# Performance work log

Hardware: AMD Instinct MI355X
Metric: run time of the kernel (lower is better)

The kernel has to match this reference:

```python
import jax, jax.numpy as jnp
import numpy as np

NUM_PTS = 1024
LATENT_SIZE = 32
BETA = 0.1


def setup_inputs() -> dict:
    key = jax.random.key(0)
    k1, k2, k3, k4 = jax.random.split(key, 4)
    B = 128
    return {
        "recon_x": jax.random.normal(k1, (B, NUM_PTS, 3), dtype=jnp.float32),
        "x": jax.random.normal(k2, (B, NUM_PTS, 3), dtype=jnp.float32),
        "mu": jax.random.normal(k3, (B, LATENT_SIZE), dtype=jnp.float32),
        "logvar": jax.random.normal(k4, (B, LATENT_SIZE), dtype=jnp.float32),
    }


def _chamfer(recon_x, x):
    # Batched squared pairwise distances: P[b, i, j] = ||x[b,i] - recon_x[b,j]||^2
    xx = jnp.sum(x * x, axis=-1)              # [B, N]
    yy = jnp.sum(recon_x * recon_x, axis=-1)  # [B, N]
    xy = jnp.einsum("bnd,bmd->bnm", x, recon_x)  # [B, N, N]
    P = xx[:, :, None] + yy[:, None, :] - 2.0 * xy
    # Bidirectional min + sum
    loss_1 = jnp.sum(jnp.min(P, axis=1))  # for each recon point, nearest x point
    loss_2 = jnp.sum(jnp.min(P, axis=2))  # for each x point, nearest recon point
    return loss_1 + loss_2


def reference(recon_x, x, mu, logvar):
    RE = _chamfer(recon_x, x) / NUM_PTS
    KLD = -0.5 * jnp.sum(1.0 + logvar - mu * mu - jnp.exp(logvar))
    KLD = KLD / LATENT_SIZE
    return RE + KLD * BETA
```

## Files before the change

kernel.cpp:

```cpp
#include <hip/hip_runtime.h>

#define NUM_PTS 1024
#define NBATCH 128
#define BT 512
#define NW 8
#define QW 128
#define R 8
#define CHAMF_SCALE (1.0f / 1024.0f)
#define KLD_SCALE   (-0.5f * 0.1f / 32.0f)

__global__ __launch_bounds__(BT, 4) void chamfer_fused(
    const float* __restrict__ recon_x,
    const float* __restrict__ x,
    float* __restrict__ ws)
{
    const int bid = blockIdx.x;
    const int dir = bid & 1;
    const int b   = (bid >> 1) & 127;
    const int rh  = bid >> 8;
    const int w   = threadIdx.x >> 6;
    const int lt  = threadIdx.x & 63;

    __shared__ float sq[NW][4][QW];
    __shared__ float comb[NW][BT];
    __shared__ float red[NW];

    {
        const float* qsrc = (dir == 0 ? recon_x : x)
            + (size_t)b * NUM_PTS * 3 + (size_t)(w * QW) * 3;
#pragma unroll
        for (int i = 0; i < 2; ++i) {
            const int p = i * 64 + lt;
            const float qx = qsrc[3 * p + 0];
            const float qy = qsrc[3 * p + 1];
            const float qz = qsrc[3 * p + 2];
            sq[w][0][p] = qx;
            sq[w][1][p] = qy;
            sq[w][2][p] = qz;
            sq[w][3][p] = fmaf(qx, qx, fmaf(qy, qy, qz * qz));
        }
    }

    const float* rp = (dir == 0 ? x : recon_x)
        + (size_t)b * NUM_PTS * 3 + (size_t)rh * 512 * 3;
    float vx[R], vy[R], vz[R], m[R];
    {
        float buf[24];
        const float4* __restrict__ s4 = (const float4*)(rp + 24 * lt);
        float4* bp = (float4*)buf;
#pragma unroll
        for (int i = 0; i < 6; ++i) bp[i] = s4[i];
#pragma unroll
        for (int k = 0; k < R; ++k) {
            vx[k] = -2.0f * buf[3 * k + 0];
            vy[k] = -2.0f * buf[3 * k + 1];
            vz[k] = -2.0f * buf[3 * k + 2];
            m[k]  = 1e30f;
        }
    }

    const float4* __restrict__ qxp = (const float4*)sq[w][0];
    const float4* __restrict__ qyp = (const float4*)sq[w][1];
    const float4* __restrict__ qzp = (const float4*)sq[w][2];
    const float4* __restrict__ q2p = (const float4*)sq[w][3];
#pragma unroll 2
    for (int g = 0; g < QW / 4; ++g) {
        const float4 qx = qxp[g];
        const float4 qy = qyp[g];
        const float4 qz = qzp[g];
        const float4 q2 = q2p[g];
#pragma unroll
        for (int r = 0; r < R; ++r) {
            const float d0 = fmaf(vx[r], qx.x, fmaf(vy[r], qy.x, fmaf(vz[r], qz.x, q2.x)));
            const float d1 = fmaf(vx[r], qx.y, fmaf(vy[r], qy.y, fmaf(vz[r], qz.y, q2.y)));
            m[r] = fminf(fminf(m[r], d0), d1);
        }
#pragma unroll
        for (int r = 0; r < R; ++r) {
            const float d2 = fmaf(vx[r], qx.z, fmaf(vy[r], qy.z, fmaf(vz[r], qz.z, q2.z)));
            const float d3 = fmaf(vx[r], qx.w, fmaf(vy[r], qy.w, fmaf(vz[r], qz.w, q2.w)));
            m[r] = fminf(fminf(m[r], d2), d3);
        }
    }

#pragma unroll
    for (int k = 0; k < R; ++k) {
        const float r2 = 0.25f * fmaf(vx[k], vx[k], fmaf(vy[k], vy[k], vz[k] * vz[k]));
        comb[w][8 * lt + k] = m[k] + r2;
    }
    __syncthreads();

    const int t = threadIdx.x;
    float v = comb[0][t];
#pragma unroll
    for (int ww = 1; ww < NW; ++ww) v = fminf(v, comb[ww][t]);

    for (int off = 32; off > 0; off >>= 1)
        v += __shfl_down(v, off, 64);
    if (lt == 0) red[w] = v;
    __syncthreads();
    if (t == 0) {
        float s = 0.0f;
#pragma unroll
        for (int ww = 0; ww < NW; ++ww) s += red[ww];
        ws[bid] = s;
    }
}

__global__ __launch_bounds__(BT) void final_reduce(
    const float* __restrict__ ws,
    const float* __restrict__ mu,
    const float* __restrict__ logvar,
    float* __restrict__ out)
{
    const int t = threadIdx.x;
    float v = ws[t] * CHAMF_SCALE;

    const float4* mp = (const float4*)mu + 2 * t;
    const float4* lp = (const float4*)logvar + 2 * t;
    float kv = 0.0f;
#pragma unroll
    for (int i = 0; i < 2; ++i) {
        const float4 mm = mp[i];
        const float4 lv = lp[i];
        kv += (1.0f + lv.x - mm.x * mm.x - expf(lv.x));
        kv += (1.0f + lv.y - mm.y * mm.y - expf(lv.y));
        kv += (1.0f + lv.z - mm.z * mm.z - expf(lv.z));
        kv += (1.0f + lv.w - mm.w * mm.w - expf(lv.w));
    }
    v += kv * KLD_SCALE;

    for (int off = 32; off > 0; off >>= 1)
        v += __shfl_down(v, off, 64);

    __shared__ float red[BT / 64];
    if ((t & 63) == 0) red[t >> 6] = v;
    __syncthreads();
    if (t == 0) {
        float s = 0.0f;
#pragma unroll
        for (int ww = 0; ww < BT / 64; ++ww) s += red[ww];
        out[0] = s;
    }
}

extern "C" void kernel_launch(void* const* d_in, const int* in_sizes, int n_in,
                              void* d_out, int out_size, void* d_ws, size_t ws_size,
                              hipStream_t stream) {
    const float* recon_x = (const float*)d_in[0];
    const float* x       = (const float*)d_in[1];
    const float* mu      = (const float*)d_in[2];
    const float* logvar  = (const float*)d_in[3];
    float* out = (float*)d_out;
    float* ws  = (float*)d_ws;

    chamfer_fused<<<512, BT, 0, stream>>>(recon_x, x, ws);
    final_reduce<<<1, BT, 0, stream>>>(ws, mu, logvar, out);
}
```

Baseline: 80.12 us.

## Compute both chamfer directions from one distance pass using rotating column minima

```diff
diff --git a/kernel.cpp b/kernel.cpp
--- a/kernel.cpp
+++ b/kernel.cpp
@@ -6,44 +6,47 @@
 #define NW 8
 #define QW 128
 #define R 8
+#define NSTEP 64
 #define CHAMF_SCALE (1.0f / 1024.0f)
 #define KLD_SCALE   (-0.5f * 0.1f / 32.0f)
 
-__global__ __launch_bounds__(BT, 4) void chamfer_fused(
+#define COL_OFF 0
+#define RS_OFF  (256 * 1024)
+#define WS2_OFF (RS_OFF + 256)
+
+__global__ __launch_bounds__(BT, 4) void chamfer_shared(
     const float* __restrict__ recon_x,
     const float* __restrict__ x,
     float* __restrict__ ws)
 {
     const int bid = blockIdx.x;
-    const int dir = bid & 1;
-    const int b   = (bid >> 1) & 127;
-    const int rh  = bid >> 8;
+    const int b   = bid >> 1;
+    const int rh  = bid & 1;
     const int w   = threadIdx.x >> 6;
     const int lt  = threadIdx.x & 63;
+    const int t   = threadIdx.x;
 
-    __shared__ float sq[NW][4][QW];
-    __shared__ float comb[NW][BT];
-    __shared__ float red[NW];
+    __shared__ float4 ring[NW][2][2 * NSTEP];
+    __shared__ float  comb[NW][BT];
+    __shared__ float  red[NW];
 
     {
-        const float* qsrc = (dir == 0 ? recon_x : x)
-            + (size_t)b * NUM_PTS * 3 + (size_t)(w * QW) * 3;
+        const float* qsrc = recon_x + (size_t)b * NUM_PTS * 3 + (size_t)(w * QW) * 3;
 #pragma unroll
         for (int i = 0; i < 2; ++i) {
-            const int p = i * 64 + lt;
-            const float qx = qsrc[3 * p + 0];
-            const float qy = qsrc[3 * p + 1];
-            const float qz = qsrc[3 * p + 2];
-            sq[w][0][p] = qx;
-            sq[w][1][p] = qy;
-            sq[w][2][p] = qz;
-            sq[w][3][p] = fmaf(qx, qx, fmaf(qy, qy, qz * qz));
+            const int c = i * 64 + lt;
+            const float qx = qsrc[3 * c + 0];
+            const float qy = qsrc[3 * c + 1];
+            const float qz = qsrc[3 * c + 2];
+            const float4 q4 = make_float4(qx, qy, qz,
+                                          fmaf(qx, qx, fmaf(qy, qy, qz * qz)));
+            ring[w][i][lt]      = q4;
+            ring[w][i][lt + 64] = q4;
         }
     }
 
-    const float* rp = (dir == 0 ? x : recon_x)
-        + (size_t)b * NUM_PTS * 3 + (size_t)rh * 512 * 3;
-    float vx[R], vy[R], vz[R], m[R];
+    const float* rp = x + (size_t)b * NUM_PTS * 3 + (size_t)rh * 512 * 3;
+    float vx[R], vy[R], vz[R], r2[R], m[R];
     {
         float buf[24];
         const float4* __restrict__ s4 = (const float4*)(rp + 24 * lt);
@@ -55,93 +58,121 @@
             vx[k] = -2.0f * buf[3 * k + 0];
             vy[k] = -2.0f * buf[3 * k + 1];
             vz[k] = -2.0f * buf[3 * k + 2];
+            r2[k] = 0.25f * fmaf(vx[k], vx[k], fmaf(vy[k], vy[k], vz[k] * vz[k]));
             m[k]  = 1e30f;
         }
     }
 
-    const float4* __restrict__ qxp = (const float4*)sq[w][0];
-    const float4* __restrict__ qyp = (const float4*)sq[w][1];
-    const float4* __restrict__ qzp = (const float4*)sq[w][2];
-    const float4* __restrict__ q2p = (const float4*)sq[w][3];
-#pragma unroll 2
-    for (int g = 0; g < QW / 4; ++g) {
-        const float4 qx = qxp[g];
-        const float4 qy = qyp[g];
-        const float4 qz = qzp[g];
-        const float4 q2 = q2p[g];
+    const float4* __restrict__ r0 = &ring[w][0][lt];
+    const float4* __restrict__ r1 = &ring[w][1][lt];
+    float ca = 1e30f, cb = 1e30f;
+    const int rotaddr = ((lt + 1) & 63) << 2;
+
+#pragma unroll 16
+    for (int s = 0; s < NSTEP; ++s) {
+        const float4 qa = r0[s];
+        const float4 qb = r1[s];
+        float da[R], db[R];
 #pragma unroll
         for (int r = 0; r < R; ++r) {
-            const float d0 = fmaf(vx[r], qx.x, fmaf(vy[r], qy.x, fmaf(vz[r], qz.x, q2.x)));
-            const float d1 = fmaf(vx[r], qx.y, fmaf(vy[r], qy.y, fmaf(vz[r], qz.y, q2.y)));
-            m[r] = fminf(fminf(m[r], d0), d1);
+            da[r] = fmaf(vx[r], qa.x, fmaf(vy[r], qa.y, fmaf(vz[r], qa.z, r2[r] + qa.w)));
+            db[r] = fmaf(vx[r], qb.x, fmaf(vy[r], qb.y, fmaf(vz[r], qb.z, r2[r] + qb.w)));
         }
 #pragma unroll
-        for (int r = 0; r < R; ++r) {
-            const float d2 = fmaf(vx[r], qx.z, fmaf(vy[r], qy.z, fmaf(vz[r], qz.z, q2.z)));
-            const float d3 = fmaf(vx[r], qx.w, fmaf(vy[r], qy.w, fmaf(vz[r], qz.w, q2.w)));
-            m[r] = fminf(fminf(m[r], d2), d3);
+        for (int r = 0; r < R; ++r)
+            m[r] = fminf(fminf(m[r], da[r]), db[r]);
+        {
+            const float t0 = fminf(fminf(da[0], da[1]), da[2]);
+            const float t1 = fminf(fminf(da[3], da[4]), da[5]);
+            const float t2 = fminf(fminf(da[6], da[7]), ca);
+            ca = fminf(fminf(t0, t1), t2);
         }
+        {
+            const float u0 = fminf(fminf(db[0], db[1]), db[2]);
+            const float u1 = fminf(fminf(db[3], db[4]), db[5]);
+            const float u2 = fminf(fminf(db[6], db[7]), cb);
+            cb = fminf(fminf(u0, u1), u2);
+        }
+        ca = __int_as_float(__builtin_amdgcn_ds_bpermute(rotaddr, __float_as_int(ca)));
+        cb = __int_as_float(__builtin_amdgcn_ds_bpermute(rotaddr, __float_as_int(cb)));
+    }
+
+    {
+        float* cp = ws + COL_OFF + (size_t)bid * 1024 + w * QW;
+        cp[lt]      = ca;
+        cp[64 + lt] = cb;
     }
 
 #pragma unroll
-    for (int k = 0; k < R; ++k) {
-        const float r2 = 0.25f * fmaf(vx[k], vx[k], fmaf(vy[k], vy[k], vz[k] * vz[k]));
-        comb[w][8 * lt + k] = m[k] + r2;
-    }
+    for (int k = 0; k < R; ++k)
+        comb[w][R * lt + k] = m[k];
     __syncthreads();
 
-    const int t = threadIdx.x;
     float v = comb[0][t];
 #pragma unroll
     for (int ww = 1; ww < NW; ++ww) v = fminf(v, comb[ww][t]);
-
     for (int off = 32; off > 0; off >>= 1)
         v += __shfl_down(v, off, 64);
     if (lt == 0) red[w] = v;
     __syncthreads();
     if (t == 0) {
-        float s = 0.0f;
+        float s = 0.f;
 #pragma unroll
         for (int ww = 0; ww < NW; ++ww) s += red[ww];
-        ws[bid] = s;
+        ws[RS_OFF + bid] = s;
     }
 }
 
-__global__ __launch_bounds__(BT) void final_reduce(
+__global__ __launch_bounds__(256) void colfold(float* __restrict__ ws)
+{
+    const int b = blockIdx.x;
+    const int t = threadIdx.x;
+    const float4* p0 = (const float4*)(ws + COL_OFF + (size_t)(2 * b)     * 1024) + t;
+    const float4* p1 = (const float4*)(ws + COL_OFF + (size_t)(2 * b + 1) * 1024) + t;
+    const float4 a = *p0;
+    const float4 c = *p1;
+    float v = fminf(a.x, c.x) + fminf(a.y, c.y) + fminf(a.z, c.z) + fminf(a.w, c.w);
+    for (int off = 32; off > 0; off >>= 1)
+        v += __shfl_down(v, off, 64);
+    __shared__ float red[4];
+    if ((t & 63) == 0) red[t >> 6] = v;
+    __syncthreads();
+    if (t == 0) {
+        float s = red[0] + red[1] + red[2] + red[3];
+        s += ws[RS_OFF + 2 * b] + ws[RS_OFF + 2 * b + 1];
+        ws[WS2_OFF + b] = s;
+    }
+}
+
+__global__ __launch_bounds__(128) void final_k(
     const float* __restrict__ ws,
     const float* __restrict__ mu,
     const float* __restrict__ logvar,
     float* __restrict__ out)
 {
     const int t = threadIdx.x;
-    float v = ws[t] * CHAMF_SCALE;
+    float v = ws[WS2_OFF + t] * CHAMF_SCALE;
 
-    const float4* mp = (const float4*)mu + 2 * t;
-    const float4* lp = (const float4*)logvar + 2 * t;
-    float kv = 0.0f;
+    const float4* mp = (const float4*)mu + 8 * t;
+    const float4* lp = (const float4*)logvar + 8 * t;
+    float kv = 0.f;
 #pragma unroll
-    for (int i = 0; i < 2; ++i) {
+    for (int i = 0; i < 8; ++i) {
         const float4 mm = mp[i];
         const float4 lv = lp[i];
-        kv += (1.0f + lv.x - mm.x * mm.x - expf(lv.x));
-        kv += (1.0f + lv.y - mm.y * mm.y - expf(lv.y));
-        kv += (1.0f + lv.z - mm.z * mm.z - expf(lv.z));
-        kv += (1.0f + lv.w - mm.w * mm.w - expf(lv.w));
+        kv += (1.f + lv.x - mm.x * mm.x - expf(lv.x));
+        kv += (1.f + lv.y - mm.y * mm.y - expf(lv.y));
+        kv += (1.f + lv.z - mm.z * mm.z - expf(lv.z));
+        kv += (1.f + lv.w - mm.w * mm.w - expf(lv.w));
     }
     v += kv * KLD_SCALE;
 
     for (int off = 32; off > 0; off >>= 1)
         v += __shfl_down(v, off, 64);
-
-    __shared__ float red[BT / 64];
+    __shared__ float red[2];
     if ((t & 63) == 0) red[t >> 6] = v;
     __syncthreads();
-    if (t == 0) {
-        float s = 0.0f;
-#pragma unroll
-        for (int ww = 0; ww < BT / 64; ++ww) s += red[ww];
-        out[0] = s;
-    }
+    if (t == 0) out[0] = red[0] + red[1];
 }
 
 extern "C" void kernel_launch(void* const* d_in, const int* in_sizes, int n_in,
@@ -154,6 +185,7 @@
     float* out = (float*)d_out;
     float* ws  = (float*)d_ws;
 
-    chamfer_fused<<<512, BT, 0, stream>>>(recon_x, x, ws);
-    final_reduce<<<1, BT, 0, stream>>>(ws, mu, logvar, out);
+    chamfer_shared<<<2 * NBATCH, BT, 0, stream>>>(recon_x, x, ws);
+    colfold<<<NBATCH, 256, 0, stream>>>(ws);
+    final_k<<<1, 128, 0, stream>>>(ws, mu, logvar, out);
 }
```

Result: no change. 78.73 us (-1.7%).
